# Performance work log

Hardware: AMD Instinct MI355X
Metric: run time of the kernel (lower is better)

The kernel has to match this reference:

```python
import jax, jax.numpy as jnp
import numpy as np

K_TOP = 2  # top-k experts per token


def setup_inputs() -> dict:
    key = jax.random.key(0)
    k1, k2, k3 = jax.random.split(key, 3)
    B, S, H, E = 4, 2048, 1024, 8
    hidden_states = jax.random.normal(k1, (B, S, H), dtype=jnp.float32)
    router_w = jax.random.normal(k2, (E, H), dtype=jnp.float32) * 0.02
    expert_weights = jax.random.normal(k3, (E, H, H), dtype=jnp.float32) * 0.02
    return {"hidden_states": hidden_states, "router_w": router_w, "expert_weights": expert_weights}


def reference(hidden_states, router_w, expert_weights):
    B, S, H = hidden_states.shape
    x = hidden_states.reshape(-1, H)                      # [N, H], N = B*S
    logits = x @ router_w.T                               # [N, E]
    probs = jax.nn.softmax(logits, axis=-1)               # [N, E]
    topk_vals, topk_idx = jax.lax.top_k(probs, K_TOP)     # [N, K]
    topk_w = topk_vals / (topk_vals.sum(-1, keepdims=True) + 1e-6)  # [N, K]

    # Dense per-expert GEMM over all tokens (single-device dispatch = identity)
    expert_out = jnp.einsum('nh,eho->eno', x, expert_weights)  # [E, N, H]

    # all_to_all_combine: gather each token's K expert outputs
    combined = jnp.take_along_axis(
        expert_out.transpose(1, 0, 2),                    # [N, E, H]
        topk_idx[:, :, None], axis=1)                     # [N, K, H]
    combined = combined.transpose(1, 0, 2)                # [K, N, H]

    # remap bias: sum over last dim of one-hot(topk_idx) * router_prob == gathered prob
    remap_bias = jnp.take_along_axis(probs, topk_idx, axis=1).T[:, :, None]  # [K, N, 1]

    weights = topk_w.T[:, :, None]                        # [K, N, 1]
    out = ((combined + remap_bias) * weights).sum(axis=0) # [N, H]
    return out.reshape(B, S, H)
```

## Files before the change

kernel.cpp:

```cpp
#include <hip/hip_runtime.h>
#include <hip/hip_fp16.h>
#include <cstdint>

typedef unsigned short u16;
typedef __attribute__((ext_vector_type(8))) short short8;
typedef __attribute__((ext_vector_type(4))) float float4v;

#define NTOK 8192
#define HDIM 1024
#define NEXP 8
#define TM 128
#define TN 128
#define BK 64
#define MAXT 136
#define WBLK 8192
#define RBLK 2048

__device__ __forceinline__ u16 f2bf(float f) {
    union { float f; uint32_t u; } v; v.f = f;
    uint32_t u = v.u;
    return (u16)((u + 0x7FFFu + ((u >> 16) & 1u)) >> 16);
}

__device__ __forceinline__ void gll16(const u16* g, u16* l) {
    __builtin_amdgcn_global_load_lds(
        (const __attribute__((address_space(1))) uint32_t*)g,
        (__attribute__((address_space(3))) uint32_t*)l,
        16, 0, 0);
}

__global__ __launch_bounds__(256) void prep(const float* __restrict__ x,
                                            const float* __restrict__ rw,
                                            const float* __restrict__ ew,
                                            u16* __restrict__ x_bf,
                                            u16* __restrict__ w_bf,
                                            float* __restrict__ wt0,
                                            float* __restrict__ wt1,
                                            float* __restrict__ biasv,
                                            int* __restrict__ sel,
                                            int* __restrict__ ctrl) {
    if (blockIdx.x == 0 && threadIdx.x < 132) ctrl[threadIdx.x] = 0;

    if (blockIdx.x < WBLK) {
        __shared__ float tile[32][33];
        const int bid = blockIdx.x;
        const int e  = bid >> 10;
        const int k0 = (bid & 31) * 32;
        const int n0 = ((bid >> 5) & 31) * 32;
        const int r = threadIdx.x >> 3;
        const int c = (threadIdx.x & 7) * 4;
        const float4 v = *(const float4*)(ew + ((size_t)e << 20) + (size_t)(k0 + r) * HDIM + n0 + c);
        tile[r][c] = v.x; tile[r][c+1] = v.y; tile[r][c+2] = v.z; tile[r][c+3] = v.w;
        __syncthreads();
        ushort4 o;
        o.x = f2bf(tile[c][r]); o.y = f2bf(tile[c+1][r]);
        o.z = f2bf(tile[c+2][r]); o.w = f2bf(tile[c+3][r]);
        *(ushort4*)(w_bf + ((size_t)e << 20) + (size_t)(n0 + r) * HDIM + k0 + c) = o;
    } else {
        const int wv = threadIdx.x >> 6;
        const int l  = threadIdx.x & 63;
        const int n  = (blockIdx.x - WBLK) * 4 + wv;
        const float4* xr = (const float4*)(x + (size_t)n * HDIM);
        ushort4* xo = (ushort4*)(x_bf + (size_t)n * HDIM);

        float4 xv[4];
#pragma unroll
        for (int t = 0; t < 4; t++) {
            xv[t] = xr[t * 64 + l];
            ushort4 p;
            p.x = f2bf(xv[t].x); p.y = f2bf(xv[t].y);
            p.z = f2bf(xv[t].z); p.w = f2bf(xv[t].w);
            xo[t * 64 + l] = p;
        }

        float logits[NEXP];
#pragma unroll
        for (int e = 0; e < NEXP; e++) {
            const float4* rwe = (const float4*)(rw + e * HDIM);
            float acc = 0.f;
#pragma unroll
            for (int t = 0; t < 4; t++) {
                const float4 r = rwe[t * 64 + l];
                acc += xv[t].x * r.x + xv[t].y * r.y + xv[t].z * r.z + xv[t].w * r.w;
            }
#pragma unroll
            for (int s = 32; s > 0; s >>= 1) acc += __shfl_xor(acc, s, 64);
            logits[e] = acc;
        }

        if (l == 0) {
            float mx = logits[0];
#pragma unroll
            for (int e = 1; e < NEXP; e++) mx = fmaxf(mx, logits[e]);
            float p[NEXP]; float sum = 0.f;
#pragma unroll
            for (int e = 0; e < NEXP; e++) { p[e] = expf(logits[e] - mx); sum += p[e]; }
            const float inv = 1.f / sum;
#pragma unroll
            for (int e = 0; e < NEXP; e++) p[e] *= inv;
            int e0 = 0;
#pragma unroll
            for (int e = 1; e < NEXP; e++) if (p[e] > p[e0]) e0 = e;
            int e1 = (e0 == 0) ? 1 : 0;
#pragma unroll
            for (int e = 0; e < NEXP; e++) if (e != e0 && p[e] > p[e1]) e1 = e;
            const float p0 = p[e0], p1 = p[e1];
            const float wsum = p0 + p1 + 1e-6f;
            const float w0 = p0 / wsum, w1 = p1 / wsum;
            wt0[n] = w0; wt1[n] = w1;
            biasv[n] = w0 * p0 + w1 * p1;
            sel[n] = e0 | (e1 << 8);
        }
    }
}

__global__ __launch_bounds__(256) void build_lists(const int* __restrict__ sel,
                                                   int* __restrict__ lists,
                                                   int* __restrict__ ctrl,
                                                   int* __restrict__ tmap) {
    const int n  = blockIdx.x * 256 + threadIdx.x;
    const int wv = threadIdx.x >> 6;
    const int l  = threadIdx.x & 63;
    const int s  = sel[n];
    const int e0 = s & 0xFF, e1 = s >> 8;
    __shared__ int wcnt[NEXP][4];
    __shared__ int ebase[NEXP];
    int pf0 = 0, pf1 = 0;
    const unsigned long long ltmask = (1ULL << l) - 1ULL;
#pragma unroll
    for (int e = 0; e < NEXP; e++) {
        const int slot = (e0 == e) ? 0 : ((e1 == e) ? 1 : -1);
        const unsigned long long bal = __ballot(slot >= 0);
        const int pf = __popcll(bal & ltmask);
        if (slot == 0) pf0 = pf;
        if (slot == 1) pf1 = pf;
        if (l == 0) wcnt[e][wv] = __popcll(bal);
    }
    __syncthreads();
    if (threadIdx.x < NEXP) {
        const int e = threadIdx.x;
        const int tot = wcnt[e][0] + wcnt[e][1] + wcnt[e][2] + wcnt[e][3];
        ebase[e] = atomicAdd(&ctrl[e * 16], tot);
    }
    __syncthreads();
    int off0 = ebase[e0], off1 = ebase[e1];
#pragma unroll
    for (int i = 0; i < 4; i++) {
        off0 += (i < wv) ? wcnt[e0][i] : 0;
        off1 += (i < wv) ? wcnt[e1][i] : 0;
    }
    lists[e0 * NTOK + off0 + pf0] = n;
    lists[e1 * NTOK + off1 + pf1] = n | 0x10000;

    __shared__ int lastflag;
    __threadfence();
    if (threadIdx.x == 0) lastflag = (atomicAdd(&ctrl[128], 1) == (int)gridDim.x - 1);
    __syncthreads();
    if (lastflag) {
        __shared__ int tbase[NEXP + 1];
        if (threadIdx.x == 0) {
            int acc = 0;
            for (int e = 0; e < NEXP; e++) {
                tbase[e] = acc;
                acc += (atomicAdd(&ctrl[e * 16], 0) + TM - 1) / TM;
            }
            tbase[NEXP] = acc;
        }
        __syncthreads();
        for (int i = threadIdx.x; i < MAXT; i += 256) {
            int v = -1;
#pragma unroll
            for (int e = 0; e < NEXP; e++)
                if (i >= tbase[e] && i < tbase[e + 1]) v = (e << 16) | (i - tbase[e]);
            tmap[i] = v;
        }
    }
}

__global__ __launch_bounds__(256) void moe_gemm(const u16* __restrict__ x_bf,
                                                const u16* __restrict__ wt_bf,
                                                const int* __restrict__ lists,
                                                const int* __restrict__ ctrl,
                                                const int* __restrict__ tmap,
                                                const float* __restrict__ wt0,
                                                const float* __restrict__ wt1,
                                                const float* __restrict__ biasv,
                                                __half* __restrict__ stage0,
                                                __half* __restrict__ stage1) {
    const int ent = tmap[blockIdx.y];
    if (ent < 0) return;
    const int e = ent >> 16;
    const int tile_m = (ent & 0xFFFF) * TM;
    const int cnt = ctrl[e * 16];
    const int tn = blockIdx.x * TN;

    __shared__ u16 lA[TM * BK];
    __shared__ u16 lB[TN * BK];
    __shared__ int   toks[TM];
    __shared__ float wgt[TM];
    __shared__ float bia[TM];
    __shared__ int   slt[TM];

    const int t  = threadIdx.x;
    const int wv = t >> 6;
    const int l  = t & 63;

    if (t < TM) {
        const int idx = tile_m + t;
        int tok = 0; float w = 0.f, b = 0.f; int sl = 0;
        if (idx < cnt) {
            const int entry = lists[e * NTOK + idx];
            tok = entry & 0xFFFF;
            sl = entry >> 16;
            w = sl ? wt1[tok] : wt0[tok];
            b = sl ? 0.f : biasv[tok];
        }
        toks[t] = tok; wgt[t] = w; bia[t] = b; slt[t] = sl;
    }
    __syncthreads();

    const int r_in = l >> 3;
    const int koff = (((l & 7) ^ r_in)) * 8;
    const u16* pA[4]; const u16* pB[4]; u16* qA[4]; u16* qB[4];
#pragma unroll
    for (int i = 0; i < 4; i++) {
        const int c = wv * 4 + i;
        const int row = c * 8 + r_in;
        pA[i] = x_bf + (size_t)toks[row] * HDIM + koff;
        pB[i] = wt_bf + ((size_t)e << 20) + (size_t)(tn + row) * HDIM + koff;
        qA[i] = lA + c * 512;
        qB[i] = lB + c * 512;
    }

    const int wm = (wv & 1) * 64;
    const int wn = (wv >> 1) * 64;
    const int fm = l & 15;
    const int fq = l >> 4;
    int aoff[4], boff[4];
#pragma unroll
    for (int i = 0; i < 4; i++) {
        const int ra = wm + i * 16 + fm;
        const int rb = wn + i * 16 + fm;
        aoff[i] = ra * 64 + ((fq ^ (ra & 7)) * 8);
        boff[i] = rb * 64 + ((fq ^ (rb & 7)) * 8);
    }

    float4v acc[4][4];
#pragma unroll
    for (int i = 0; i < 4; i++)
#pragma unroll
        for (int j = 0; j < 4; j++) { float4v z = {0.f, 0.f, 0.f, 0.f}; acc[i][j] = z; }

    for (int k0 = 0; k0 < HDIM; k0 += BK) {
        __syncthreads();
#pragma unroll
        for (int i = 0; i < 4; i++) {
            gll16(pA[i] + k0, qA[i]);
            gll16(pB[i] + k0, qB[i]);
        }
        __syncthreads();

#pragma unroll
        for (int kh = 0; kh < 2; kh++) {
            short8 af[4], bf[4];
#pragma unroll
            for (int mf = 0; mf < 4; mf++)
                af[mf] = *(const short8*)&lA[aoff[mf] ^ (kh << 5)];
#pragma unroll
            for (int nf = 0; nf < 4; nf++)
                bf[nf] = *(const short8*)&lB[boff[nf] ^ (kh << 5)];
#pragma unroll
            for (int mf = 0; mf < 4; mf++)
#pragma unroll
                for (int nf = 0; nf < 4; nf++)
                    acc[mf][nf] = __builtin_amdgcn_mfma_f32_16x16x32_bf16(af[mf], bf[nf], acc[mf][nf], 0, 0, 0);
        }
    }

#pragma unroll
    for (int mf = 0; mf < 4; mf++) {
#pragma unroll
        for (int r = 0; r < 4; r++) {
            const int m_local = wm + mf * 16 + fq * 4 + r;
            if (tile_m + m_local < cnt) {
                const int tok = toks[m_local];
                const float w = wgt[m_local], b = bia[m_local];
                __half* sp = (slt[m_local] ? stage1 : stage0) + (size_t)tok * HDIM;
#pragma unroll
                for (int nf = 0; nf < 4; nf++) {
                    const int h = tn + wn + nf * 16 + fm;
                    sp[h] = __float2half(acc[mf][nf][r] * w + b);
                }
            }
        }
    }
}

__global__ __launch_bounds__(256) void combine(const __half* __restrict__ s0,
                                               const __half* __restrict__ s1,
                                               float* __restrict__ out) {
    const size_t idx = ((size_t)blockIdx.x * 256 + threadIdx.x) * 8;
    union { uint4 v; __half h[8]; } a, b;
    a.v = *(const uint4*)(s0 + idx);
    b.v = *(const uint4*)(s1 + idx);
    float4 o0, o1;
    o0.x = __half2float(a.h[0]) + __half2float(b.h[0]);
    o0.y = __half2float(a.h[1]) + __half2float(b.h[1]);
    o0.z = __half2float(a.h[2]) + __half2float(b.h[2]);
    o0.w = __half2float(a.h[3]) + __half2float(b.h[3]);
    o1.x = __half2float(a.h[4]) + __half2float(b.h[4]);
    o1.y = __half2float(a.h[5]) + __half2float(b.h[5]);
    o1.z = __half2float(a.h[6]) + __half2float(b.h[6]);
    o1.w = __half2float(a.h[7]) + __half2float(b.h[7]);
    *(float4*)(out + idx)     = o0;
    *(float4*)(out + idx + 4) = o1;
}

extern "C" void kernel_launch(void* const* d_in, const int* in_sizes, int n_in,
                              void* d_out, int out_size, void* d_ws, size_t ws_size,
                              hipStream_t stream) {
    const float* x  = (const float*)d_in[0];
    const float* rw = (const float*)d_in[1];
    const float* ew = (const float*)d_in[2];
    float* out = (float*)d_out;

    char* ws = (char*)d_ws;
    u16*    x_bf   = (u16*)ws;
    u16*    w_bf   = (u16*)(ws + 16777216);
    __half* stage0 = (__half*)(ws + 33554432);
    __half* stage1 = (__half*)(ws + 50331648);
    float*  wt0    = (float*)(ws + 67108864);
    float*  wt1    = (float*)(ws + 67141632);
    float*  biasv  = (float*)(ws + 67174400);
    int*    sel    = (int*)(ws + 67207168);
    int*    lists  = (int*)(ws + 67239936);
    int*    ctrl   = (int*)(ws + 67502080);
    int*    tmap   = (int*)(ws + 67502720);

    prep<<<WBLK + RBLK, 256, 0, stream>>>(x, rw, ew, x_bf, w_bf, wt0, wt1, biasv, sel, ctrl);
    build_lists<<<NTOK / 256, 256, 0, stream>>>(sel, lists, ctrl, tmap);
    moe_gemm<<<dim3(HDIM / TN, MAXT, 1), 256, 0, stream>>>(
        x_bf, w_bf, lists, ctrl, tmap, wt0, wt1, biasv, stage0, stage1);
    combine<<<(NTOK * HDIM) / (256 * 8), 256, 0, stream>>>(stage0, stage1, out);
}
```

Before: 201.6 us.

## Double-buffer LDS tiles in MoE GEMM and swap grid axes

The MoE GEMM now keeps two LDS buffers for the A and B tiles. It issues the async global-to-LDS loads for the next K step before running the MFMAs on the current one, which cuts the two barriers per iteration down to one and aims to hide load latency behind compute. It also swaps the grid axes so the tile-map index runs along x and the N tile along y, which changes block scheduling order and the L2 reuse of weights. LDS use per block doubles to about 64KB, which may lower occupancy. There is also a possible race, because the next-buffer loads are issued with no wait before the single barrier (global_load_lds completion relies on vmcnt).

```diff
diff --git a/kernel.cpp b/kernel.cpp
--- a/kernel.cpp
+++ b/kernel.cpp
@@ -15,6 +15,7 @@
 #define MAXT 136
 #define WBLK 8192
 #define RBLK 2048
+#define ABUF (TM * BK)
 
 __device__ __forceinline__ u16 f2bf(float f) {
     union { float f; uint32_t u; } v; v.f = f;
@@ -187,15 +188,15 @@
                                                 const float* __restrict__ biasv,
                                                 __half* __restrict__ stage0,
                                                 __half* __restrict__ stage1) {
-    const int ent = tmap[blockIdx.y];
+    const int ent = tmap[blockIdx.x];
     if (ent < 0) return;
     const int e = ent >> 16;
     const int tile_m = (ent & 0xFFFF) * TM;
     const int cnt = ctrl[e * 16];
-    const int tn = blockIdx.x * TN;
-
-    __shared__ u16 lA[TM * BK];
-    __shared__ u16 lB[TN * BK];
+    const int tn = blockIdx.y * TN;
+
+    __shared__ u16 lA[2 * ABUF];
+    __shared__ u16 lB[2 * ABUF];
     __shared__ int   toks[TM];
     __shared__ float wgt[TM];
     __shared__ float bia[TM];
@@ -221,15 +222,14 @@
 
     const int r_in = l >> 3;
     const int koff = (((l & 7) ^ r_in)) * 8;
-    const u16* pA[4]; const u16* pB[4]; u16* qA[4]; u16* qB[4];
+    const u16* pA[4]; const u16* pB[4]; int qoff[4];
 #pragma unroll
     for (int i = 0; i < 4; i++) {
         const int c = wv * 4 + i;
         const int row = c * 8 + r_in;
         pA[i] = x_bf + (size_t)toks[row] * HDIM + koff;
         pB[i] = wt_bf + ((size_t)e << 20) + (size_t)(tn + row) * HDIM + koff;
-        qA[i] = lA + c * 512;
-        qB[i] = lB + c * 512;
+        qoff[i] = c * 512;
     }
 
     const int wm = (wv & 1) * 64;
@@ -251,29 +251,45 @@
 #pragma unroll
         for (int j = 0; j < 4; j++) { float4v z = {0.f, 0.f, 0.f, 0.f}; acc[i][j] = z; }
 
+#pragma unroll
+    for (int i = 0; i < 4; i++) {
+        gll16(pA[i], lA + qoff[i]);
+        gll16(pB[i], lB + qoff[i]);
+    }
+    int p = 0;
+    __syncthreads();
+
     for (int k0 = 0; k0 < HDIM; k0 += BK) {
-        __syncthreads();
-#pragma unroll
-        for (int i = 0; i < 4; i++) {
-            gll16(pA[i] + k0, qA[i]);
-            gll16(pB[i] + k0, qB[i]);
-        }
-        __syncthreads();
-
+        const int nk = k0 + BK;
+        if (nk < HDIM) {
+            const int pb = (p ^ 1) * ABUF;
+#pragma unroll
+            for (int i = 0; i < 4; i++) {
+                gll16(pA[i] + nk, lA + pb + qoff[i]);
+                gll16(pB[i] + nk, lB + pb + qoff[i]);
+            }
+        }
+
+        const int cb = p * ABUF;
 #pragma unroll
         for (int kh = 0; kh < 2; kh++) {
             short8 af[4], bf[4];
 #pragma unroll
             for (int mf = 0; mf < 4; mf++)
-                af[mf] = *(const short8*)&lA[aoff[mf] ^ (kh << 5)];
+                af[mf] = *(const short8*)&lA[cb + (aoff[mf] ^ (kh << 5))];
 #pragma unroll
             for (int nf = 0; nf < 4; nf++)
-                bf[nf] = *(const short8*)&lB[boff[nf] ^ (kh << 5)];
+                bf[nf] = *(const short8*)&lB[cb + (boff[nf] ^ (kh << 5))];
 #pragma unroll
             for (int mf = 0; mf < 4; mf++)
 #pragma unroll
                 for (int nf = 0; nf < 4; nf++)
                     acc[mf][nf] = __builtin_amdgcn_mfma_f32_16x16x32_bf16(af[mf], bf[nf], acc[mf][nf], 0, 0, 0);
+        }
+
+        if (nk < HDIM) {
+            __syncthreads();
+            p ^= 1;
         }
     }
 
@@ -339,7 +355,7 @@
 
     prep<<<WBLK + RBLK, 256, 0, stream>>>(x, rw, ew, x_bf, w_bf, wt0, wt1, biasv, sel, ctrl);
     build_lists<<<NTOK / 256, 256, 0, stream>>>(sel, lists, ctrl, tmap);
-    moe_gemm<<<dim3(HDIM / TN, MAXT, 1), 256, 0, stream>>>(
+    moe_gemm<<<dim3(MAXT, HDIM / TN, 1), 256, 0, stream>>>(
         x_bf, w_bf, lists, ctrl, tmap, wt0, wt1, biasv, stage0, stage1);
     combine<<<(NTOK * HDIM) / (256 * 8), 256, 0, stream>>>(stage0, stage1, out);
 }
```

Measured after the change: 207.8 us. 1.03x slower.

## Triple-buffer LDS with async prefetch and swap grid axes in MoE GEMM

Applied to the files above, without the earlier changes.

Replaces the single-buffered BK=64 loop, which had two barriers per step, with a three-slot LDS ring at BK=32. The next K slice is prefetched via global_load_lds before computing the current one, and a single vmcnt wait plus barrier is used per iteration. The grid axes are also swapped so consecutive blocks walk token tiles rather than N tiles, which changes the L2 reuse pattern for expert weights versus activations. The tradeoffs are twice as many iterations with half the MFMA work per barrier, plus a hand-written waitcnt that must match the compiler's load accounting.

```diff
diff --git a/kernel.cpp b/kernel.cpp
--- a/kernel.cpp
+++ b/kernel.cpp
@@ -11,7 +11,9 @@
 #define NEXP 8
 #define TM 128
 #define TN 128
-#define BK 64
+#define BK 32
+#define NITER (HDIM / BK)
+#define ABUF (TM * BK)
 #define MAXT 136
 #define WBLK 8192
 #define RBLK 2048
@@ -187,15 +189,15 @@
                                                 const float* __restrict__ biasv,
                                                 __half* __restrict__ stage0,
                                                 __half* __restrict__ stage1) {
-    const int ent = tmap[blockIdx.y];
+    const int ent = tmap[blockIdx.x];
     if (ent < 0) return;
     const int e = ent >> 16;
     const int tile_m = (ent & 0xFFFF) * TM;
     const int cnt = ctrl[e * 16];
-    const int tn = blockIdx.x * TN;
-
-    __shared__ u16 lA[TM * BK];
-    __shared__ u16 lB[TN * BK];
+    const int tn = blockIdx.y * TN;
+
+    __shared__ u16 lA[3 * ABUF];
+    __shared__ u16 lB[3 * ABUF];
     __shared__ int   toks[TM];
     __shared__ float wgt[TM];
     __shared__ float bia[TM];
@@ -219,17 +221,16 @@
     }
     __syncthreads();
 
-    const int r_in = l >> 3;
-    const int koff = (((l & 7) ^ r_in)) * 8;
-    const u16* pA[4]; const u16* pB[4]; u16* qA[4]; u16* qB[4];
-#pragma unroll
-    for (int i = 0; i < 4; i++) {
-        const int c = wv * 4 + i;
-        const int row = c * 8 + r_in;
+    const int r_in = l >> 2;
+    const int koff = ((l & 3) ^ (r_in & 3)) * 8;
+    const u16* pA[2]; const u16* pB[2]; int qoff[2];
+#pragma unroll
+    for (int i = 0; i < 2; i++) {
+        const int c = wv * 2 + i;
+        const int row = c * 16 + r_in;
         pA[i] = x_bf + (size_t)toks[row] * HDIM + koff;
         pB[i] = wt_bf + ((size_t)e << 20) + (size_t)(tn + row) * HDIM + koff;
-        qA[i] = lA + c * 512;
-        qB[i] = lB + c * 512;
+        qoff[i] = c * 512;
     }
 
     const int wm = (wv & 1) * 64;
@@ -241,8 +242,8 @@
     for (int i = 0; i < 4; i++) {
         const int ra = wm + i * 16 + fm;
         const int rb = wn + i * 16 + fm;
-        aoff[i] = ra * 64 + ((fq ^ (ra & 7)) * 8);
-        boff[i] = rb * 64 + ((fq ^ (rb & 7)) * 8);
+        aoff[i] = ra * 32 + ((fq ^ (ra & 3)) * 8);
+        boff[i] = rb * 32 + ((fq ^ (rb & 3)) * 8);
     }
 
     float4v acc[4][4];
@@ -251,30 +252,41 @@
 #pragma unroll
         for (int j = 0; j < 4; j++) { float4v z = {0.f, 0.f, 0.f, 0.f}; acc[i][j] = z; }
 
-    for (int k0 = 0; k0 < HDIM; k0 += BK) {
-        __syncthreads();
-#pragma unroll
-        for (int i = 0; i < 4; i++) {
-            gll16(pA[i] + k0, qA[i]);
-            gll16(pB[i] + k0, qB[i]);
-        }
-        __syncthreads();
-
-#pragma unroll
-        for (int kh = 0; kh < 2; kh++) {
-            short8 af[4], bf[4];
-#pragma unroll
-            for (int mf = 0; mf < 4; mf++)
-                af[mf] = *(const short8*)&lA[aoff[mf] ^ (kh << 5)];
+    gll16(pA[0], lA + qoff[0]);
+    gll16(pA[1], lA + qoff[1]);
+    gll16(pB[0], lB + qoff[0]);
+    gll16(pB[1], lB + qoff[1]);
+
+    int cur = 0, nxt = 1;
+    for (int it = 0; it < NITER; ++it) {
+        if (it < NITER - 1) {
+            const int nk = (it + 1) * BK;
+            u16* la = lA + nxt * ABUF;
+            u16* lb = lB + nxt * ABUF;
+            gll16(pA[0] + nk, la + qoff[0]);
+            gll16(pA[1] + nk, la + qoff[1]);
+            gll16(pB[0] + nk, lb + qoff[0]);
+            gll16(pB[1] + nk, lb + qoff[1]);
+            asm volatile("s_waitcnt vmcnt(4)\n\ts_barrier" ::: "memory");
+        } else {
+            asm volatile("s_waitcnt vmcnt(0)\n\ts_barrier" ::: "memory");
+        }
+
+        const u16* ca = lA + cur * ABUF;
+        const u16* cb = lB + cur * ABUF;
+        short8 af[4], bf[4];
+#pragma unroll
+        for (int mf = 0; mf < 4; mf++) af[mf] = *(const short8*)&ca[aoff[mf]];
+#pragma unroll
+        for (int nf = 0; nf < 4; nf++) bf[nf] = *(const short8*)&cb[boff[nf]];
+#pragma unroll
+        for (int mf = 0; mf < 4; mf++)
 #pragma unroll
             for (int nf = 0; nf < 4; nf++)
-                bf[nf] = *(const short8*)&lB[boff[nf] ^ (kh << 5)];
-#pragma unroll
-            for (int mf = 0; mf < 4; mf++)
-#pragma unroll
-                for (int nf = 0; nf < 4; nf++)
-                    acc[mf][nf] = __builtin_amdgcn_mfma_f32_16x16x32_bf16(af[mf], bf[nf], acc[mf][nf], 0, 0, 0);
-        }
+                acc[mf][nf] = __builtin_amdgcn_mfma_f32_16x16x32_bf16(af[mf], bf[nf], acc[mf][nf], 0, 0, 0);
+
+        cur = nxt;
+        nxt = (nxt == 2) ? 0 : nxt + 1;
     }
 
 #pragma unroll
@@ -339,7 +351,7 @@
 
     prep<<<WBLK + RBLK, 256, 0, stream>>>(x, rw, ew, x_bf, w_bf, wt0, wt1, biasv, sel, ctrl);
     build_lists<<<NTOK / 256, 256, 0, stream>>>(sel, lists, ctrl, tmap);
-    moe_gemm<<<dim3(HDIM / TN, MAXT, 1), 256, 0, stream>>>(
+    moe_gemm<<<dim3(MAXT, HDIM / TN, 1), 256, 0, stream>>>(
         x_bf, w_bf, lists, ctrl, tmap, wt0, wt1, biasv, stage0, stage1);
     combine<<<(NTOK * HDIM) / (256 * 8), 256, 0, stream>>>(stage0, stage1, out);
 }
```

Result: no change. 198.8 us (-1.4%).
